# Optimization experiments

Measured on AMD Instinct MI355X. Metric: run time of the kernel, lower is better.

Reference implementation:

```python
import jax, jax.numpy as jnp
import numpy as np

B, T, C = 2, 4096, 768
H = 12
D = C // H  # head_dim = 64

def setup_inputs() -> dict:
    key = jax.random.key(0)
    ks = jax.random.split(key, 5)
    s = 1.0 / np.sqrt(C)
    return {
        "x": jax.random.normal(ks[0], (B, T, C), dtype=jnp.float32),
        "qkv_w": jax.random.normal(ks[1], (C, 3 * C), dtype=jnp.float32) * s,
        "qkv_b": jax.random.normal(ks[2], (3 * C,), dtype=jnp.float32) * 0.02,
        "out_w": jax.random.normal(ks[3], (C, C), dtype=jnp.float32) * s,
        "out_b": jax.random.normal(ks[4], (C,), dtype=jnp.float32) * 0.02,
    }

def reference(x, qkv_w, qkv_b, out_w, out_b):
    b, t, c = x.shape
    qkv = x @ qkv_w + qkv_b                      # [B,T,3C]
    q, k, v = jnp.split(qkv, 3, axis=-1)
    # [B,T,C] -> [B,H,T,D]
    q = q.reshape(b, t, H, D).transpose(0, 2, 1, 3)
    k = k.reshape(b, t, H, D).transpose(0, 2, 1, 3)
    v = v.reshape(b, t, H, D).transpose(0, 2, 1, 3)
    scale = 1.0 / np.sqrt(D)
    attn = jnp.einsum('bhqd,bhkd->bhqk', q, k) * scale  # [B,H,T,T]
    causal = jnp.tril(jnp.ones((t, t), dtype=bool))
    attn = jnp.where(causal, attn, -jnp.inf)
    attn = jax.nn.softmax(attn, axis=-1)
    y = jnp.einsum('bhqk,bhkd->bhqd', attn, v)           # [B,H,T,D]
    y = y.transpose(0, 2, 1, 3).reshape(b, t, c)
    return y @ out_w + out_b
```

## Files before the change

kernel.cpp:

```cpp
#include <hip/hip_runtime.h>
#include <hip/hip_bf16.h>

#define T_SEQ 4096
#define C_DIM 768
#define H_NUM 12
#define D_HEAD 64
#define N3    2304
#define BHN   24

typedef __bf16 bf16x8 __attribute__((ext_vector_type(8)));
typedef float  f32x4  __attribute__((ext_vector_type(4)));

__device__ inline unsigned short f2b(float f) {
    unsigned int x = __float_as_uint(f);
    unsigned int r = (x + 0x7FFFu + ((x >> 16) & 1u)) >> 16;
    return (unsigned short)r;
}

__device__ inline unsigned int pack_trunc(float lo, float hi) {
    return __builtin_amdgcn_perm(__float_as_uint(hi), __float_as_uint(lo), 0x07060302u);
}

__device__ inline void load_lds16(const unsigned short* g, unsigned short* l) {
    __builtin_amdgcn_global_load_lds(
        (const __attribute__((address_space(1))) unsigned int*)(g),
        (__attribute__((address_space(3))) unsigned int*)(l),
        16, 0, 0);
}

__device__ inline void transpose_tile(const float* __restrict__ in,
                                      unsigned short* __restrict__ out,
                                      unsigned short* Ts, int k0, int n0,
                                      int R, int Cc, int tid)
{
    #pragma unroll
    for (int it = 0; it < 4; ++it) {
        int idx = tid + it * 256;
        int r = idx >> 4, c4 = idx & 15;
        float4 v = *reinterpret_cast<const float4*>(&in[(size_t)(k0 + r) * Cc + n0 + c4 * 4]);
        Ts[(c4 * 4 + 0) * 72 + r] = f2b(v.x);
        Ts[(c4 * 4 + 1) * 72 + r] = f2b(v.y);
        Ts[(c4 * 4 + 2) * 72 + r] = f2b(v.z);
        Ts[(c4 * 4 + 3) * 72 + r] = f2b(v.w);
    }
    __syncthreads();
    #pragma unroll
    for (int it = 0; it < 2; ++it) {
        int idx = tid + it * 256;
        int row = idx >> 3, ch = idx & 7;
        *reinterpret_cast<uint4*>(&out[(size_t)(n0 + row) * R + k0 + ch * 8]) =
            *reinterpret_cast<const uint4*>(&Ts[row * 72 + ch * 8]);
    }
}

__global__ __launch_bounds__(256) void prep(
    const float* __restrict__ x, const float* __restrict__ qkv_w,
    const float* __restrict__ out_w,
    unsigned short* __restrict__ xb, unsigned short* __restrict__ wtq,
    unsigned short* __restrict__ wto)
{
    __shared__ unsigned short Ts[64 * 72];
    const int b = blockIdx.x, tid = threadIdx.x;
    if (b < 6144) {
        int idx = b * 256 + tid;
        float4 v = reinterpret_cast<const float4*>(x)[idx];
        ushort4 u;
        u.x = f2b(v.x); u.y = f2b(v.y); u.z = f2b(v.z); u.w = f2b(v.w);
        reinterpret_cast<ushort4*>(xb)[idx] = u;
    } else if (b < 6576) {
        int bb = b - 6144;
        transpose_tile(qkv_w, wtq, Ts, (bb % 12) * 64, (bb / 12) * 64, C_DIM, N3, tid);
    } else {
        int bb = b - 6576;
        transpose_tile(out_w, wto, Ts, (bb % 12) * 64, (bb / 12) * 64, C_DIM, C_DIM, tid);
    }
}

__global__ __launch_bounds__(256) void qkv_gemm(
    const unsigned short* __restrict__ xb, const unsigned short* __restrict__ wt,
    const float* __restrict__ bias,
    unsigned short* __restrict__ Q, unsigned short* __restrict__ K,
    unsigned short* __restrict__ Vt)
{
    __shared__ unsigned short SH[128 * 128];
    unsigned short* As = SH;
    unsigned short* Bs = SH + 128 * 64;
    const int tid  = threadIdx.x;
    const int m0   = blockIdx.x * 128;
    const int n0   = blockIdx.y * 128;
    const int lane = tid & 63;
    const int wv   = tid >> 6;
    const int wr   = wv >> 1, wc = wv & 1;
    const int quad = lane >> 4;
    const int lr   = lane & 15;
    const int srow = lane >> 3;
    const int dch  = (lane & 7) ^ srow;

    f32x4 acc[4][4] = {};

    for (int kk = 0; kk < C_DIM; kk += 64) {
        __syncthreads();
        #pragma unroll
        for (int i = 0; i < 4; ++i) {
            int inst = wv * 4 + i;
            int r = inst * 8 + srow;
            load_lds16(xb + (size_t)(m0 + r) * C_DIM + kk + dch * 8, As + inst * 512);
            load_lds16(wt + (size_t)(n0 + r) * C_DIM + kk + dch * 8, Bs + inst * 512);
        }
        __syncthreads();
        #pragma unroll
        for (int k2 = 0; k2 < 2; ++k2) {
            bf16x8 af[4], bf[4];
            #pragma unroll
            for (int mt = 0; mt < 4; ++mt)
                af[mt] = *reinterpret_cast<const bf16x8*>(
                    &As[(wr * 64 + mt * 16 + lr) * 64 + (((k2 * 4 + quad) ^ (lr & 7)) * 8)]);
            #pragma unroll
            for (int nt = 0; nt < 4; ++nt)
                bf[nt] = *reinterpret_cast<const bf16x8*>(
                    &Bs[(wc * 64 + nt * 16 + lr) * 64 + (((k2 * 4 + quad) ^ (lr & 7)) * 8)]);
            #pragma unroll
            for (int mt = 0; mt < 4; ++mt)
                #pragma unroll
                for (int nt = 0; nt < 4; ++nt)
                    acc[mt][nt] = __builtin_amdgcn_mfma_f32_16x16x32_bf16(af[mt], bf[nt], acc[mt][nt], 0, 0, 0);
        }
    }

    const int whichblk = n0 / C_DIM;
    if (whichblk == 2) {
        __syncthreads();
        #pragma unroll
        for (int nt = 0; nt < 4; ++nt) {
            int dp = wc * 64 + nt * 16 + lr;
            float bj = bias[n0 + dp];
            #pragma unroll
            for (int mt = 0; mt < 4; ++mt) {
                int t0 = wr * 64 + mt * 16 + quad * 4;
                ushort4 u;
                u.x = f2b(acc[mt][nt][0] + bj);
                u.y = f2b(acc[mt][nt][1] + bj);
                u.z = f2b(acc[mt][nt][2] + bj);
                u.w = f2b(acc[mt][nt][3] + bj);
                int cs = (t0 >> 2) ^ ((dp & 15) << 1);
                *reinterpret_cast<ushort4*>(&SH[dp * 128 + cs * 4]) = u;
            }
        }
        __syncthreads();
        const int bb = m0 >> 12;
        const int t_base = m0 & 4095;
        const int h_base = (n0 - 2 * C_DIM) >> 6;
        #pragma unroll
        for (int i = 0; i < 8; ++i) {
            int idx = i * 256 + tid;
            int row = idx >> 4, cc = idx & 15;
            int pc = ((2 * cc) ^ ((row & 15) << 1)) * 4;
            uint4 val = *reinterpret_cast<const uint4*>(&SH[row * 128 + pc]);
            int head = h_base + (row >> 6);
            int d = row & 63;
            *reinterpret_cast<uint4*>(
                &Vt[((size_t)(bb * H_NUM + head) * D_HEAD + d) * T_SEQ + t_base + cc * 8]) = val;
        }
    } else {
        const int head0 = ((n0 % C_DIM) + wc * 64) >> 6;
        #pragma unroll
        for (int nt = 0; nt < 4; ++nt) {
            int d = nt * 16 + lr;
            float bj = bias[n0 + wc * 64 + nt * 16 + lr];
            #pragma unroll
            for (int mt = 0; mt < 4; ++mt) {
                #pragma unroll
                for (int reg = 0; reg < 4; ++reg) {
                    int i = m0 + wr * 64 + mt * 16 + quad * 4 + reg;
                    int bb = i >> 12, t = i & 4095;
                    float val = acc[mt][nt][reg] + bj;
                    size_t base = (size_t)(bb * H_NUM + head0) * T_SEQ + t;
                    if (whichblk == 0)
                        Q[base * D_HEAD + d] = f2b(val * 0.18033688011f);
                    else
                        K[base * D_HEAD + d] = f2b(val);
                }
            }
        }
    }
}

__global__ __launch_bounds__(256, 3) void flash_attn(
    const unsigned short* __restrict__ Q, const unsigned short* __restrict__ K,
    const unsigned short* __restrict__ Vt, unsigned short* __restrict__ Y)
{
    __shared__ unsigned short Ks[2][64 * 64];
    __shared__ unsigned short Vs[2][64 * 64];
    __shared__ unsigned short Ps[2][64 * 72];
    const int tid  = threadIdx.x;
    const int lane = tid & 63;
    const int wv   = tid >> 6;
    const int quad = lane >> 4;
    const int lr   = lane & 15;
    const int srow = lane >> 3;
    const int dch  = (lane & 7) ^ srow;

    const int bid = blockIdx.x;
    const int qt  = 31 - (bid / BHN);
    const int bh  = bid % BHN;
    const int q0  = qt * 128;
    const int diag0 = 2 * qt;
    const int last  = diag0 + 1;

    const unsigned short* Qb = Q  + (size_t)bh * T_SEQ * D_HEAD;
    const unsigned short* Kb = K  + (size_t)bh * T_SEQ * D_HEAD;
    const unsigned short* Vb = Vt + (size_t)bh * D_HEAD * T_SEQ;

    bf16x8 bQ[2][2];
    #pragma unroll
    for (int h = 0; h < 2; ++h)
        #pragma unroll
        for (int k2 = 0; k2 < 2; ++k2)
            bQ[h][k2] = *reinterpret_cast<const bf16x8*>(
                &Qb[(size_t)(q0 + h * 64 + wv * 16 + lr) * D_HEAD + k2 * 32 + quad * 8]);

    bf16x8 ones;
    #pragma unroll
    for (int i = 0; i < 8; ++i) ones[i] = (__bf16)1.0f;
    const f32x4 zf = {};

    f32x4 oacc[2][4] = {};
    f32x4 lacc[2] = {};

    unsigned short* Pw0 = &Ps[0][(wv * 16) * 72];
    unsigned short* Pw1 = &Ps[1][(wv * 16) * 72];

    #pragma unroll
    for (int i = 0; i < 2; ++i) {
        int inst = wv * 2 + i;
        int r = inst * 8 + srow;
        load_lds16(Kb + (size_t)r * D_HEAD + dch * 8, Ks[0] + inst * 512);
        load_lds16(Vb + (size_t)r * T_SEQ + dch * 8, Vs[0] + inst * 512);
    }

    for (int kt = 0; kt <= last; ++kt) {
        const int buf = kt & 1;
        __syncthreads();

        if (kt < last) {
            #pragma unroll
            for (int i = 0; i < 2; ++i) {
                int inst = wv * 2 + i;
                int r = inst * 8 + srow;
                load_lds16(Kb + (size_t)((kt + 1) * 64 + r) * D_HEAD + dch * 8,
                           Ks[buf ^ 1] + inst * 512);
                load_lds16(Vb + (size_t)r * T_SEQ + (kt + 1) * 64 + dch * 8,
                           Vs[buf ^ 1] + inst * 512);
            }
        }

        const bool doh0 = (kt <= diag0);

        bf16x8 aK[4][2];
        #pragma unroll
        for (int mt = 0; mt < 4; ++mt)
            #pragma unroll
            for (int k2 = 0; k2 < 2; ++k2)
                aK[mt][k2] = *reinterpret_cast<const bf16x8*>(
                    &Ks[buf][(mt * 16 + lr) * 64 + (((k2 * 4 + quad) ^ (lr & 7)) * 8)]);

        f32x4 st0[4], st1[4];
        #pragma unroll
        for (int mt = 0; mt < 4; ++mt) {
            st1[mt] = __builtin_amdgcn_mfma_f32_16x16x32_bf16(aK[mt][0], bQ[1][0], zf, 0, 0, 0);
            st1[mt] = __builtin_amdgcn_mfma_f32_16x16x32_bf16(aK[mt][1], bQ[1][1], st1[mt], 0, 0, 0);
        }
        if (doh0) {
            #pragma unroll
            for (int mt = 0; mt < 4; ++mt) {
                st0[mt] = __builtin_amdgcn_mfma_f32_16x16x32_bf16(aK[mt][0], bQ[0][0], zf, 0, 0, 0);
                st0[mt] = __builtin_amdgcn_mfma_f32_16x16x32_bf16(aK[mt][1], bQ[0][1], st0[mt], 0, 0, 0);
            }
        }

        if (kt == diag0) {
            int qg = q0 + wv * 16 + lr;
            #pragma unroll
            for (int mt = 0; mt < 4; ++mt)
                #pragma unroll
                for (int reg = 0; reg < 4; ++reg)
                    if (kt * 64 + mt * 16 + quad * 4 + reg > qg) st0[mt][reg] = -INFINITY;
        }
        if (kt == last) {
            int qg = q0 + 64 + wv * 16 + lr;
            #pragma unroll
            for (int mt = 0; mt < 4; ++mt)
                #pragma unroll
                for (int reg = 0; reg < 4; ++reg)
                    if (kt * 64 + mt * 16 + quad * 4 + reg > qg) st1[mt][reg] = -INFINITY;
        }

        #pragma unroll
        for (int mt = 0; mt < 4; ++mt) {
            #pragma unroll
            for (int reg = 0; reg < 4; ++reg)
                st1[mt][reg] = __builtin_amdgcn_exp2f(st1[mt][reg]);
            uint2 u;
            u.x = pack_trunc(st1[mt][0], st1[mt][1]);
            u.y = pack_trunc(st1[mt][2], st1[mt][3]);
            *reinterpret_cast<uint2*>(&Pw1[lr * 72 + mt * 16 + quad * 4]) = u;
        }
        if (doh0) {
            #pragma unroll
            for (int mt = 0; mt < 4; ++mt) {
                #pragma unroll
                for (int reg = 0; reg < 4; ++reg)
                    st0[mt][reg] = __builtin_amdgcn_exp2f(st0[mt][reg]);
                uint2 u;
                u.x = pack_trunc(st0[mt][0], st0[mt][1]);
                u.y = pack_trunc(st0[mt][2], st0[mt][3]);
                *reinterpret_cast<uint2*>(&Pw0[lr * 72 + mt * 16 + quad * 4]) = u;
            }
        }

        bf16x8 aV[4][2];
        #pragma unroll
        for (int mt = 0; mt < 4; ++mt)
            #pragma unroll
            for (int k2 = 0; k2 < 2; ++k2)
                aV[mt][k2] = *reinterpret_cast<const bf16x8*>(
                    &Vs[buf][(mt * 16 + lr) * 64 + (((k2 * 4 + quad) ^ (lr & 7)) * 8)]);

        if (doh0) {
            bf16x8 bP0 = *reinterpret_cast<const bf16x8*>(&Pw0[lr * 72 + quad * 8]);
            bf16x8 bP1 = *reinterpret_cast<const bf16x8*>(&Pw0[lr * 72 + 32 + quad * 8]);
            #pragma unroll
            for (int dt = 0; dt < 4; ++dt) {
                oacc[0][dt] = __builtin_amdgcn_mfma_f32_16x16x32_bf16(aV[dt][0], bP0, oacc[0][dt], 0, 0, 0);
                oacc[0][dt] = __builtin_amdgcn_mfma_f32_16x16x32_bf16(aV[dt][1], bP1, oacc[0][dt], 0, 0, 0);
            }
            lacc[0] = __builtin_amdgcn_mfma_f32_16x16x32_bf16(ones, bP0, lacc[0], 0, 0, 0);
            lacc[0] = __builtin_amdgcn_mfma_f32_16x16x32_bf16(ones, bP1, lacc[0], 0, 0, 0);
        }
        {
            bf16x8 bP0 = *reinterpret_cast<const bf16x8*>(&Pw1[lr * 72 + quad * 8]);
            bf16x8 bP1 = *reinterpret_cast<const bf16x8*>(&Pw1[lr * 72 + 32 + quad * 8]);
            #pragma unroll
            for (int dt = 0; dt < 4; ++dt) {
                oacc[1][dt] = __builtin_amdgcn_mfma_f32_16x16x32_bf16(aV[dt][0], bP0, oacc[1][dt], 0, 0, 0);
                oacc[1][dt] = __builtin_amdgcn_mfma_f32_16x16x32_bf16(aV[dt][1], bP1, oacc[1][dt], 0, 0, 0);
            }
            lacc[1] = __builtin_amdgcn_mfma_f32_16x16x32_bf16(ones, bP0, lacc[1], 0, 0, 0);
            lacc[1] = __builtin_amdgcn_mfma_f32_16x16x32_bf16(ones, bP1, lacc[1], 0, 0, 0);
        }
    }

    const int bb = bh / H_NUM, hh = bh % H_NUM;
    #pragma unroll
    for (int h = 0; h < 2; ++h) {
        float inv = 1.f / lacc[h][0];
        int q = q0 + h * 64 + wv * 16 + lr;
        #pragma unroll
        for (int dt = 0; dt < 4; ++dt) {
            ushort4 u;
            u.x = f2b(oacc[h][dt][0] * inv);
            u.y = f2b(oacc[h][dt][1] * inv);
            u.z = f2b(oacc[h][dt][2] * inv);
            u.w = f2b(oacc[h][dt][3] * inv);
            *reinterpret_cast<ushort4*>(
                &Y[(size_t)(bb * T_SEQ + q) * C_DIM + hh * 64 + dt * 16 + quad * 4]) = u;
        }
    }
}

__global__ __launch_bounds__(256) void out_gemm(
    const unsigned short* __restrict__ Y, const unsigned short* __restrict__ wt,
    const float* __restrict__ bias, float* __restrict__ out)
{
    __shared__ unsigned short As[128 * 64];
    __shared__ unsigned short Bs[64 * 64];
    const int tid  = threadIdx.x;
    const int m0   = blockIdx.x * 128;
    const int n0   = blockIdx.y * 64;
    const int lane = tid & 63;
    const int wv   = tid >> 6;
    const int wr   = wv >> 1, wc = wv & 1;
    const int quad = lane >> 4;
    const int lr   = lane & 15;
    const int srow = lane >> 3;
    const int dch  = (lane & 7) ^ srow;

    f32x4 acc[4][2] = {};

    for (int kk = 0; kk < C_DIM; kk += 64) {
        __syncthreads();
        #pragma unroll
        for (int i = 0; i < 4; ++i) {
            int inst = wv * 4 + i;
            int r = inst * 8 + srow;
            load_lds16(Y + (size_t)(m0 + r) * C_DIM + kk + dch * 8, As + inst * 512);
        }
        #pragma unroll
        for (int i = 0; i < 2; ++i) {
            int inst = wv * 2 + i;
            int r = inst * 8 + srow;
            load_lds16(wt + (size_t)(n0 + r) * C_DIM + kk + dch * 8, Bs + inst * 512);
        }
        __syncthreads();
        #pragma unroll
        for (int k2 = 0; k2 < 2; ++k2) {
            bf16x8 af[4], bf[2];
            #pragma unroll
            for (int mt = 0; mt < 4; ++mt)
                af[mt] = *reinterpret_cast<const bf16x8*>(
                    &As[(wr * 64 + mt * 16 + lr) * 64 + (((k2 * 4 + quad) ^ (lr & 7)) * 8)]);
            #pragma unroll
            for (int nt = 0; nt < 2; ++nt)
                bf[nt] = *reinterpret_cast<const bf16x8*>(
                    &Bs[(wc * 32 + nt * 16 + lr) * 64 + (((k2 * 4 + quad) ^ (lr & 7)) * 8)]);
            #pragma unroll
            for (int mt = 0; mt < 4; ++mt)
                #pragma unroll
                for (int nt = 0; nt < 2; ++nt)
                    acc[mt][nt] = __builtin_amdgcn_mfma_f32_16x16x32_bf16(af[mt], bf[nt], acc[mt][nt], 0, 0, 0);
        }
    }

    #pragma unroll
    for (int nt = 0; nt < 2; ++nt) {
        int j = n0 + wc * 32 + nt * 16 + lr;
        float bj = bias[j];
        #pragma unroll
        for (int mt = 0; mt < 4; ++mt)
            #pragma unroll
            for (int reg = 0; reg < 4; ++reg) {
                int i = m0 + wr * 64 + mt * 16 + quad * 4 + reg;
                out[(size_t)i * C_DIM + j] = acc[mt][nt][reg] + bj;
            }
    }
}

extern "C" void kernel_launch(void* const* d_in, const int* in_sizes, int n_in,
                              void* d_out, int out_size, void* d_ws, size_t ws_size,
                              hipStream_t stream) {
    const float* x     = (const float*)d_in[0];
    const float* qkv_w = (const float*)d_in[1];
    const float* qkv_b = (const float*)d_in[2];
    const float* out_w = (const float*)d_in[3];
    const float* out_b = (const float*)d_in[4];
    float* out = (float*)d_out;

    unsigned short* xb  = (unsigned short*)d_ws;
    unsigned short* wtq = xb  + (size_t)8192 * 768;
    unsigned short* wto = wtq + (size_t)2304 * 768;
    unsigned short* Qs  = wto + (size_t)768 * 768;
    unsigned short* Kg  = Qs  + (size_t)BHN * T_SEQ * D_HEAD;
    unsigned short* Vt  = Kg  + (size_t)BHN * T_SEQ * D_HEAD;
    unsigned short* Y   = xb;

    prep      <<<6720, 256, 0, stream>>>(x, qkv_w, out_w, xb, wtq, wto);
    qkv_gemm  <<<dim3(64, 18), 256, 0, stream>>>(xb, wtq, qkv_b, Qs, Kg, Vt);
    flash_attn<<<dim3(32 * BHN), 256, 0, stream>>>(Qs, Kg, Vt, Y);
    out_gemm  <<<dim3(64, 12), 256, 0, stream>>>(Y, wto, out_b, out);
}
```

Measured before the change: 230.5 us.

## Keep P in registers using 16x16x16 MFMA, dropping LDS P round-trip

```diff
diff --git a/kernel.cpp b/kernel.cpp
--- a/kernel.cpp
+++ b/kernel.cpp
@@ -10,6 +10,7 @@
 
 typedef __bf16 bf16x8 __attribute__((ext_vector_type(8)));
 typedef float  f32x4  __attribute__((ext_vector_type(4)));
+typedef short  s16x4  __attribute__((ext_vector_type(4)));
 
 __device__ inline unsigned short f2b(float f) {
     unsigned int x = __float_as_uint(f);
@@ -185,13 +186,12 @@
     }
 }
 
-__global__ __launch_bounds__(256, 3) void flash_attn(
+__global__ __launch_bounds__(256, 4) void flash_attn(
     const unsigned short* __restrict__ Q, const unsigned short* __restrict__ K,
     const unsigned short* __restrict__ Vt, unsigned short* __restrict__ Y)
 {
     __shared__ unsigned short Ks[2][64 * 64];
     __shared__ unsigned short Vs[2][64 * 64];
-    __shared__ unsigned short Ps[2][64 * 72];
     const int tid  = threadIdx.x;
     const int lane = tid & 63;
     const int wv   = tid >> 6;
@@ -219,16 +219,13 @@
             bQ[h][k2] = *reinterpret_cast<const bf16x8*>(
                 &Qb[(size_t)(q0 + h * 64 + wv * 16 + lr) * D_HEAD + k2 * 32 + quad * 8]);
 
-    bf16x8 ones;
-    #pragma unroll
-    for (int i = 0; i < 8; ++i) ones[i] = (__bf16)1.0f;
+    s16x4 ones4;
+    #pragma unroll
+    for (int i = 0; i < 4; ++i) ones4[i] = (short)0x3F80;
     const f32x4 zf = {};
 
     f32x4 oacc[2][4] = {};
     f32x4 lacc[2] = {};
-
-    unsigned short* Pw0 = &Ps[0][(wv * 16) * 72];
-    unsigned short* Pw1 = &Ps[1][(wv * 16) * 72];
 
     #pragma unroll
     for (int i = 0; i < 2; ++i) {
@@ -256,25 +253,18 @@
 
         const bool doh0 = (kt <= diag0);
 
-        bf16x8 aK[4][2];
-        #pragma unroll
-        for (int mt = 0; mt < 4; ++mt)
-            #pragma unroll
-            for (int k2 = 0; k2 < 2; ++k2)
-                aK[mt][k2] = *reinterpret_cast<const bf16x8*>(
-                    &Ks[buf][(mt * 16 + lr) * 64 + (((k2 * 4 + quad) ^ (lr & 7)) * 8)]);
-
         f32x4 st0[4], st1[4];
         #pragma unroll
         for (int mt = 0; mt < 4; ++mt) {
-            st1[mt] = __builtin_amdgcn_mfma_f32_16x16x32_bf16(aK[mt][0], bQ[1][0], zf, 0, 0, 0);
-            st1[mt] = __builtin_amdgcn_mfma_f32_16x16x32_bf16(aK[mt][1], bQ[1][1], st1[mt], 0, 0, 0);
-        }
-        if (doh0) {
-            #pragma unroll
-            for (int mt = 0; mt < 4; ++mt) {
-                st0[mt] = __builtin_amdgcn_mfma_f32_16x16x32_bf16(aK[mt][0], bQ[0][0], zf, 0, 0, 0);
-                st0[mt] = __builtin_amdgcn_mfma_f32_16x16x32_bf16(aK[mt][1], bQ[0][1], st0[mt], 0, 0, 0);
+            bf16x8 aK0 = *reinterpret_cast<const bf16x8*>(
+                &Ks[buf][(mt * 16 + lr) * 64 + ((quad ^ (lr & 7)) * 8)]);
+            bf16x8 aK1 = *reinterpret_cast<const bf16x8*>(
+                &Ks[buf][(mt * 16 + lr) * 64 + (((4 + quad) ^ (lr & 7)) * 8)]);
+            st1[mt] = __builtin_amdgcn_mfma_f32_16x16x32_bf16(aK0, bQ[1][0], zf, 0, 0, 0);
+            st1[mt] = __builtin_amdgcn_mfma_f32_16x16x32_bf16(aK1, bQ[1][1], st1[mt], 0, 0, 0);
+            if (doh0) {
+                st0[mt] = __builtin_amdgcn_mfma_f32_16x16x32_bf16(aK0, bQ[0][0], zf, 0, 0, 0);
+                st0[mt] = __builtin_amdgcn_mfma_f32_16x16x32_bf16(aK1, bQ[0][1], st0[mt], 0, 0, 0);
             }
         }
 
@@ -295,6 +285,7 @@
                     if (kt * 64 + mt * 16 + quad * 4 + reg > qg) st1[mt][reg] = -INFINITY;
         }
 
+        s16x4 bP1v[4], bP0v[4];
         #pragma unroll
         for (int mt = 0; mt < 4; ++mt) {
             #pragma unroll
@@ -303,7 +294,7 @@
             uint2 u;
             u.x = pack_trunc(st1[mt][0], st1[mt][1]);
             u.y = pack_trunc(st1[mt][2], st1[mt][3]);
-            *reinterpret_cast<uint2*>(&Pw1[lr * 72 + mt * 16 + quad * 4]) = u;
+            bP1v[mt] = __builtin_bit_cast(s16x4, u);
         }
         if (doh0) {
             #pragma unroll
@@ -314,39 +305,28 @@
                 uint2 u;
                 u.x = pack_trunc(st0[mt][0], st0[mt][1]);
                 u.y = pack_trunc(st0[mt][2], st0[mt][3]);
-                *reinterpret_cast<uint2*>(&Pw0[lr * 72 + mt * 16 + quad * 4]) = u;
-            }
-        }
-
-        bf16x8 aV[4][2];
-        #pragma unroll
-        for (int mt = 0; mt < 4; ++mt)
-            #pragma unroll
-            for (int k2 = 0; k2 < 2; ++k2)
-                aV[mt][k2] = *reinterpret_cast<const bf16x8*>(
-                    &Vs[buf][(mt * 16 + lr) * 64 + (((k2 * 4 + quad) ^ (lr & 7)) * 8)]);
-
-        if (doh0) {
-            bf16x8 bP0 = *reinterpret_cast<const bf16x8*>(&Pw0[lr * 72 + quad * 8]);
-            bf16x8 bP1 = *reinterpret_cast<const bf16x8*>(&Pw0[lr * 72 + 32 + quad * 8]);
-            #pragma unroll
-            for (int dt = 0; dt < 4; ++dt) {
-                oacc[0][dt] = __builtin_amdgcn_mfma_f32_16x16x32_bf16(aV[dt][0], bP0, oacc[0][dt], 0, 0, 0);
-                oacc[0][dt] = __builtin_amdgcn_mfma_f32_16x16x32_bf16(aV[dt][1], bP1, oacc[0][dt], 0, 0, 0);
-            }
-            lacc[0] = __builtin_amdgcn_mfma_f32_16x16x32_bf16(ones, bP0, lacc[0], 0, 0, 0);
-            lacc[0] = __builtin_amdgcn_mfma_f32_16x16x32_bf16(ones, bP1, lacc[0], 0, 0, 0);
-        }
-        {
-            bf16x8 bP0 = *reinterpret_cast<const bf16x8*>(&Pw1[lr * 72 + quad * 8]);
-            bf16x8 bP1 = *reinterpret_cast<const bf16x8*>(&Pw1[lr * 72 + 32 + quad * 8]);
-            #pragma unroll
-            for (int dt = 0; dt < 4; ++dt) {
-                oacc[1][dt] = __builtin_amdgcn_mfma_f32_16x16x32_bf16(aV[dt][0], bP0, oacc[1][dt], 0, 0, 0);
-                oacc[1][dt] = __builtin_amdgcn_mfma_f32_16x16x32_bf16(aV[dt][1], bP1, oacc[1][dt], 0, 0, 0);
-            }
-            lacc[1] = __builtin_amdgcn_mfma_f32_16x16x32_bf16(ones, bP0, lacc[1], 0, 0, 0);
-            lacc[1] = __builtin_amdgcn_mfma_f32_16x16x32_bf16(ones, bP1, lacc[1], 0, 0, 0);
+                bP0v[mt] = __builtin_bit_cast(s16x4, u);
+            }
+        }
+
+        #pragma unroll
+        for (int kb = 0; kb < 4; ++kb) {
+            s16x4 aV[4];
+            #pragma unroll
+            for (int dt = 0; dt < 4; ++dt)
+                aV[dt] = *reinterpret_cast<const s16x4*>(
+                    &Vs[buf][(dt * 16 + lr) * 64 +
+                             (((2 * kb + (quad >> 1)) ^ (lr & 7)) * 8) + (quad & 1) * 4]);
+            #pragma unroll
+            for (int dt = 0; dt < 4; ++dt)
+                oacc[1][dt] = __builtin_amdgcn_mfma_f32_16x16x16bf16_1k(aV[dt], bP1v[kb], oacc[1][dt], 0, 0, 0);
+            lacc[1] = __builtin_amdgcn_mfma_f32_16x16x16bf16_1k(ones4, bP1v[kb], lacc[1], 0, 0, 0);
+            if (doh0) {
+                #pragma unroll
+                for (int dt = 0; dt < 4; ++dt)
+                    oacc[0][dt] = __builtin_amdgcn_mfma_f32_16x16x16bf16_1k(aV[dt], bP0v[kb], oacc[0][dt], 0, 0, 0);
+                lacc[0] = __builtin_amdgcn_mfma_f32_16x16x16bf16_1k(ones4, bP0v[kb], lacc[0], 0, 0, 0);
+            }
         }
     }
 
```

Result: slower. 240.5 us (+4.3%).

## Balance causal attention work by splitting long query tiles across blocks

Applied to the files above, without the earlier changes.

```diff
diff --git a/kernel.cpp b/kernel.cpp
--- a/kernel.cpp
+++ b/kernel.cpp
@@ -187,7 +187,8 @@
 
 __global__ __launch_bounds__(256, 3) void flash_attn(
     const unsigned short* __restrict__ Q, const unsigned short* __restrict__ K,
-    const unsigned short* __restrict__ Vt, unsigned short* __restrict__ Y)
+    const unsigned short* __restrict__ Vt, unsigned short* __restrict__ Y,
+    float* __restrict__ pO, float* __restrict__ pl)
 {
     __shared__ unsigned short Ks[2][64 * 64];
     __shared__ unsigned short Vs[2][64 * 64];
@@ -201,170 +202,239 @@
     const int dch  = (lane & 7) ^ srow;
 
     const int bid = blockIdx.x;
-    const int qt  = 31 - (bid / BHN);
+    const int ip  = bid / BHN;
     const int bh  = bid % BHN;
-    const int q0  = qt * 128;
-    const int diag0 = 2 * qt;
-    const int last  = diag0 + 1;
 
     const unsigned short* Qb = Q  + (size_t)bh * T_SEQ * D_HEAD;
     const unsigned short* Kb = K  + (size_t)bh * T_SEQ * D_HEAD;
     const unsigned short* Vb = Vt + (size_t)bh * D_HEAD * T_SEQ;
 
-    bf16x8 bQ[2][2];
-    #pragma unroll
-    for (int h = 0; h < 2; ++h)
-        #pragma unroll
-        for (int k2 = 0; k2 < 2; ++k2)
-            bQ[h][k2] = *reinterpret_cast<const bf16x8*>(
-                &Qb[(size_t)(q0 + h * 64 + wv * 16 + lr) * D_HEAD + k2 * 32 + quad * 8]);
+    int njob, jqt[2], jk0[2], jk1[2], jpart[2];
+    if (ip < 16) {
+        njob = 2;
+        jqt[0] = ip;      jk0[0] = 0; jk1[0] = 2 * ip + 2;  jpart[0] = 0;
+        jqt[1] = 31 - ip; jk0[1] = 0; jk1[1] = 31 - 2 * ip; jpart[1] = 1;
+    } else {
+        njob = 1;
+        jqt[0] = ip; jk0[0] = 2 * ip - 31; jk1[0] = 2 * ip + 2; jpart[0] = 2;
+    }
 
     bf16x8 ones;
     #pragma unroll
     for (int i = 0; i < 8; ++i) ones[i] = (__bf16)1.0f;
     const f32x4 zf = {};
 
-    f32x4 oacc[2][4] = {};
-    f32x4 lacc[2] = {};
-
     unsigned short* Pw0 = &Ps[0][(wv * 16) * 72];
     unsigned short* Pw1 = &Ps[1][(wv * 16) * 72];
-
+    const int bb = bh / H_NUM, hh = bh % H_NUM;
+
+    int buf = 0;
+    {
+        int kt = jk0[0];
+        #pragma unroll
+        for (int i = 0; i < 2; ++i) {
+            int inst = wv * 2 + i;
+            int r = inst * 8 + srow;
+            load_lds16(Kb + (size_t)(kt * 64 + r) * D_HEAD + dch * 8, Ks[0] + inst * 512);
+            load_lds16(Vb + (size_t)r * T_SEQ + kt * 64 + dch * 8, Vs[0] + inst * 512);
+        }
+    }
+
+    for (int job = 0; job < njob; ++job) {
+        const int qt = jqt[job];
+        const int q0 = qt * 128;
+        const int diag0 = 2 * qt;
+        const int lastk = 2 * qt + 1;
+        const int k0 = jk0[job], k1 = jk1[job];
+
+        bf16x8 bQ[2][2];
+        #pragma unroll
+        for (int h = 0; h < 2; ++h)
+            #pragma unroll
+            for (int k2 = 0; k2 < 2; ++k2)
+                bQ[h][k2] = *reinterpret_cast<const bf16x8*>(
+                    &Qb[(size_t)(q0 + h * 64 + wv * 16 + lr) * D_HEAD + k2 * 32 + quad * 8]);
+
+        f32x4 oacc[2][4] = {};
+        f32x4 lacc[2] = {};
+
+        for (int kt = k0; kt < k1; ++kt) {
+            __syncthreads();
+
+            int nkt = (kt + 1 < k1) ? (kt + 1) : ((job + 1 < njob) ? jk0[job + 1] : -1);
+            if (nkt >= 0) {
+                #pragma unroll
+                for (int i = 0; i < 2; ++i) {
+                    int inst = wv * 2 + i;
+                    int r = inst * 8 + srow;
+                    load_lds16(Kb + (size_t)(nkt * 64 + r) * D_HEAD + dch * 8,
+                               Ks[buf ^ 1] + inst * 512);
+                    load_lds16(Vb + (size_t)r * T_SEQ + nkt * 64 + dch * 8,
+                               Vs[buf ^ 1] + inst * 512);
+                }
+            }
+
+            const bool doh0 = (kt <= diag0);
+
+            bf16x8 aK[4][2];
+            #pragma unroll
+            for (int mt = 0; mt < 4; ++mt)
+                #pragma unroll
+                for (int k2 = 0; k2 < 2; ++k2)
+                    aK[mt][k2] = *reinterpret_cast<const bf16x8*>(
+                        &Ks[buf][(mt * 16 + lr) * 64 + (((k2 * 4 + quad) ^ (lr & 7)) * 8)]);
+
+            f32x4 st0[4], st1[4];
+            #pragma unroll
+            for (int mt = 0; mt < 4; ++mt) {
+                st1[mt] = __builtin_amdgcn_mfma_f32_16x16x32_bf16(aK[mt][0], bQ[1][0], zf, 0, 0, 0);
+                st1[mt] = __builtin_amdgcn_mfma_f32_16x16x32_bf16(aK[mt][1], bQ[1][1], st1[mt], 0, 0, 0);
+            }
+            if (doh0) {
+                #pragma unroll
+                for (int mt = 0; mt < 4; ++mt) {
+                    st0[mt] = __builtin_amdgcn_mfma_f32_16x16x32_bf16(aK[mt][0], bQ[0][0], zf, 0, 0, 0);
+                    st0[mt] = __builtin_amdgcn_mfma_f32_16x16x32_bf16(aK[mt][1], bQ[0][1], st0[mt], 0, 0, 0);
+                }
+            }
+
+            if (kt == diag0) {
+                int qg = q0 + wv * 16 + lr;
+                #pragma unroll
+                for (int mt = 0; mt < 4; ++mt)
+                    #pragma unroll
+                    for (int reg = 0; reg < 4; ++reg)
+                        if (kt * 64 + mt * 16 + quad * 4 + reg > qg) st0[mt][reg] = -INFINITY;
+            }
+            if (kt == lastk) {
+                int qg = q0 + 64 + wv * 16 + lr;
+                #pragma unroll
+                for (int mt = 0; mt < 4; ++mt)
+                    #pragma unroll
+                    for (int reg = 0; reg < 4; ++reg)
+                        if (kt * 64 + mt * 16 + quad * 4 + reg > qg) st1[mt][reg] = -INFINITY;
+            }
+
+            #pragma unroll
+            for (int mt = 0; mt < 4; ++mt) {
+                #pragma unroll
+                for (int reg = 0; reg < 4; ++reg)
+                    st1[mt][reg] = __builtin_amdgcn_exp2f(st1[mt][reg]);
+                uint2 u;
+                u.x = pack_trunc(st1[mt][0], st1[mt][1]);
+                u.y = pack_trunc(st1[mt][2], st1[mt][3]);
+                *reinterpret_cast<uint2*>(&Pw1[lr * 72 + mt * 16 + quad * 4]) = u;
+            }
+            if (doh0) {
+                #pragma unroll
+                for (int mt = 0; mt < 4; ++mt) {
+                    #pragma unroll
+                    for (int reg = 0; reg < 4; ++reg)
+                        st0[mt][reg] = __builtin_amdgcn_exp2f(st0[mt][reg]);
+                    uint2 u;
+                    u.x = pack_trunc(st0[mt][0], st0[mt][1]);
+                    u.y = pack_trunc(st0[mt][2], st0[mt][3]);
+                    *reinterpret_cast<uint2*>(&Pw0[lr * 72 + mt * 16 + quad * 4]) = u;
+                }
+            }
+
+            bf16x8 aV[4][2];
+            #pragma unroll
+            for (int mt = 0; mt < 4; ++mt)
+                #pragma unroll
+                for (int k2 = 0; k2 < 2; ++k2)
+                    aV[mt][k2] = *reinterpret_cast<const bf16x8*>(
+                        &Vs[buf][(mt * 16 + lr) * 64 + (((k2 * 4 + quad) ^ (lr & 7)) * 8)]);
+
+            if (doh0) {
+                bf16x8 bP0 = *reinterpret_cast<const bf16x8*>(&Pw0[lr * 72 + quad * 8]);
+                bf16x8 bP1 = *reinterpret_cast<const bf16x8*>(&Pw0[lr * 72 + 32 + quad * 8]);
+                #pragma unroll
+                for (int dt = 0; dt < 4; ++dt) {
+                    oacc[0][dt] = __builtin_amdgcn_mfma_f32_16x16x32_bf16(aV[dt][0], bP0, oacc[0][dt], 0, 0, 0);
+                    oacc[0][dt] = __builtin_amdgcn_mfma_f32_16x16x32_bf16(aV[dt][1], bP1, oacc[0][dt], 0, 0, 0);
+                }
+                lacc[0] = __builtin_amdgcn_mfma_f32_16x16x32_bf16(ones, bP0, lacc[0], 0, 0, 0);
+                lacc[0] = __builtin_amdgcn_mfma_f32_16x16x32_bf16(ones, bP1, lacc[0], 0, 0, 0);
+            }
+            {
+                bf16x8 bP0 = *reinterpret_cast<const bf16x8*>(&Pw1[lr * 72 + quad * 8]);
+                bf16x8 bP1 = *reinterpret_cast<const bf16x8*>(&Pw1[lr * 72 + 32 + quad * 8]);
+                #pragma unroll
+                for (int dt = 0; dt < 4; ++dt) {
+                    oacc[1][dt] = __builtin_amdgcn_mfma_f32_16x16x32_bf16(aV[dt][0], bP0, oacc[1][dt], 0, 0, 0);
+                    oacc[1][dt] = __builtin_amdgcn_mfma_f32_16x16x32_bf16(aV[dt][1], bP1, oacc[1][dt], 0, 0, 0);
+                }
+                lacc[1] = __builtin_amdgcn_mfma_f32_16x16x32_bf16(ones, bP0, lacc[1], 0, 0, 0);
+                lacc[1] = __builtin_amdgcn_mfma_f32_16x16x32_bf16(ones, bP1, lacc[1], 0, 0, 0);
+            }
+
+            buf ^= 1;
+        }
+
+        if (jpart[job] == 0) {
+            #pragma unroll
+            for (int h = 0; h < 2; ++h) {
+                float inv = 1.f / lacc[h][0];
+                int q = q0 + h * 64 + wv * 16 + lr;
+                #pragma unroll
+                for (int dt = 0; dt < 4; ++dt) {
+                    ushort4 u;
+                    u.x = f2b(oacc[h][dt][0] * inv);
+                    u.y = f2b(oacc[h][dt][1] * inv);
+                    u.z = f2b(oacc[h][dt][2] * inv);
+                    u.w = f2b(oacc[h][dt][3] * inv);
+                    *reinterpret_cast<ushort4*>(
+                        &Y[(size_t)(bb * T_SEQ + q) * C_DIM + hh * 64 + dt * 16 + quad * 4]) = u;
+                }
+            }
+        } else {
+            const int slot = jpart[job] - 1;
+            const int iH = 31 - qt;
+            const size_t s = (size_t)slot * 384 + (size_t)bh * 16 + iH;
+            float* po  = pO + s * 8192;
+            float* plp = pl + s * 128;
+            #pragma unroll
+            for (int h = 0; h < 2; ++h) {
+                int q = h * 64 + wv * 16 + lr;
+                if (quad == 0) plp[q] = lacc[h][0];
+                #pragma unroll
+                for (int dt = 0; dt < 4; ++dt)
+                    *reinterpret_cast<f32x4*>(&po[(size_t)q * 64 + dt * 16 + quad * 4]) = oacc[h][dt];
+            }
+        }
+    }
+}
+
+__global__ __launch_bounds__(256) void combine(
+    const float* __restrict__ pO, const float* __restrict__ pl,
+    unsigned short* __restrict__ Y)
+{
+    const int s   = blockIdx.x;
+    const int tid = threadIdx.x;
+    const int bh  = s / 16, iH = s % 16;
+    const int qt  = 31 - iH;
+    const int bb  = bh / H_NUM, hh = bh % H_NUM;
+    const int q0  = qt * 128;
+    const float* a  = pO + (size_t)s * 8192;
+    const float* b  = pO + (size_t)(384 + s) * 8192;
+    const float* la = pl + (size_t)s * 128;
+    const float* lb = pl + (size_t)(384 + s) * 128;
     #pragma unroll
-    for (int i = 0; i < 2; ++i) {
-        int inst = wv * 2 + i;
-        int r = inst * 8 + srow;
-        load_lds16(Kb + (size_t)r * D_HEAD + dch * 8, Ks[0] + inst * 512);
-        load_lds16(Vb + (size_t)r * T_SEQ + dch * 8, Vs[0] + inst * 512);
-    }
-
-    for (int kt = 0; kt <= last; ++kt) {
-        const int buf = kt & 1;
-        __syncthreads();
-
-        if (kt < last) {
-            #pragma unroll
-            for (int i = 0; i < 2; ++i) {
-                int inst = wv * 2 + i;
-                int r = inst * 8 + srow;
-                load_lds16(Kb + (size_t)((kt + 1) * 64 + r) * D_HEAD + dch * 8,
-                           Ks[buf ^ 1] + inst * 512);
-                load_lds16(Vb + (size_t)r * T_SEQ + (kt + 1) * 64 + dch * 8,
-                           Vs[buf ^ 1] + inst * 512);
-            }
-        }
-
-        const bool doh0 = (kt <= diag0);
-
-        bf16x8 aK[4][2];
-        #pragma unroll
-        for (int mt = 0; mt < 4; ++mt)
-            #pragma unroll
-            for (int k2 = 0; k2 < 2; ++k2)
-                aK[mt][k2] = *reinterpret_cast<const bf16x8*>(
-                    &Ks[buf][(mt * 16 + lr) * 64 + (((k2 * 4 + quad) ^ (lr & 7)) * 8)]);
-
-        f32x4 st0[4], st1[4];
-        #pragma unroll
-        for (int mt = 0; mt < 4; ++mt) {
-            st1[mt] = __builtin_amdgcn_mfma_f32_16x16x32_bf16(aK[mt][0], bQ[1][0], zf, 0, 0, 0);
-            st1[mt] = __builtin_amdgcn_mfma_f32_16x16x32_bf16(aK[mt][1], bQ[1][1], st1[mt], 0, 0, 0);
-        }
-        if (doh0) {
-            #pragma unroll
-            for (int mt = 0; mt < 4; ++mt) {
-                st0[mt] = __builtin_amdgcn_mfma_f32_16x16x32_bf16(aK[mt][0], bQ[0][0], zf, 0, 0, 0);
-                st0[mt] = __builtin_amdgcn_mfma_f32_16x16x32_bf16(aK[mt][1], bQ[0][1], st0[mt], 0, 0, 0);
-            }
-        }
-
-        if (kt == diag0) {
-            int qg = q0 + wv * 16 + lr;
-            #pragma unroll
-            for (int mt = 0; mt < 4; ++mt)
-                #pragma unroll
-                for (int reg = 0; reg < 4; ++reg)
-                    if (kt * 64 + mt * 16 + quad * 4 + reg > qg) st0[mt][reg] = -INFINITY;
-        }
-        if (kt == last) {
-            int qg = q0 + 64 + wv * 16 + lr;
-            #pragma unroll
-            for (int mt = 0; mt < 4; ++mt)
-                #pragma unroll
-                for (int reg = 0; reg < 4; ++reg)
-                    if (kt * 64 + mt * 16 + quad * 4 + reg > qg) st1[mt][reg] = -INFINITY;
-        }
-
-        #pragma unroll
-        for (int mt = 0; mt < 4; ++mt) {
-            #pragma unroll
-            for (int reg = 0; reg < 4; ++reg)
-                st1[mt][reg] = __builtin_amdgcn_exp2f(st1[mt][reg]);
-            uint2 u;
-            u.x = pack_trunc(st1[mt][0], st1[mt][1]);
-            u.y = pack_trunc(st1[mt][2], st1[mt][3]);
-            *reinterpret_cast<uint2*>(&Pw1[lr * 72 + mt * 16 + quad * 4]) = u;
-        }
-        if (doh0) {
-            #pragma unroll
-            for (int mt = 0; mt < 4; ++mt) {
-                #pragma unroll
-                for (int reg = 0; reg < 4; ++reg)
-                    st0[mt][reg] = __builtin_amdgcn_exp2f(st0[mt][reg]);
-                uint2 u;
-                u.x = pack_trunc(st0[mt][0], st0[mt][1]);
-                u.y = pack_trunc(st0[mt][2], st0[mt][3]);
-                *reinterpret_cast<uint2*>(&Pw0[lr * 72 + mt * 16 + quad * 4]) = u;
-            }
-        }
-
-        bf16x8 aV[4][2];
-        #pragma unroll
-        for (int mt = 0; mt < 4; ++mt)
-            #pragma unroll
-            for (int k2 = 0; k2 < 2; ++k2)
-                aV[mt][k2] = *reinterpret_cast<const bf16x8*>(
-                    &Vs[buf][(mt * 16 + lr) * 64 + (((k2 * 4 + quad) ^ (lr & 7)) * 8)]);
-
-        if (doh0) {
-            bf16x8 bP0 = *reinterpret_cast<const bf16x8*>(&Pw0[lr * 72 + quad * 8]);
-            bf16x8 bP1 = *reinterpret_cast<const bf16x8*>(&Pw0[lr * 72 + 32 + quad * 8]);
-            #pragma unroll
-            for (int dt = 0; dt < 4; ++dt) {
-                oacc[0][dt] = __builtin_amdgcn_mfma_f32_16x16x32_bf16(aV[dt][0], bP0, oacc[0][dt], 0, 0, 0);
-                oacc[0][dt] = __builtin_amdgcn_mfma_f32_16x16x32_bf16(aV[dt][1], bP1, oacc[0][dt], 0, 0, 0);
-            }
-            lacc[0] = __builtin_amdgcn_mfma_f32_16x16x32_bf16(ones, bP0, lacc[0], 0, 0, 0);
-            lacc[0] = __builtin_amdgcn_mfma_f32_16x16x32_bf16(ones, bP1, lacc[0], 0, 0, 0);
-        }
-        {
-            bf16x8 bP0 = *reinterpret_cast<const bf16x8*>(&Pw1[lr * 72 + quad * 8]);
-            bf16x8 bP1 = *reinterpret_cast<const bf16x8*>(&Pw1[lr * 72 + 32 + quad * 8]);
-            #pragma unroll
-            for (int dt = 0; dt < 4; ++dt) {
-                oacc[1][dt] = __builtin_amdgcn_mfma_f32_16x16x32_bf16(aV[dt][0], bP0, oacc[1][dt], 0, 0, 0);
-                oacc[1][dt] = __builtin_amdgcn_mfma_f32_16x16x32_bf16(aV[dt][1], bP1, oacc[1][dt], 0, 0, 0);
-            }
-            lacc[1] = __builtin_amdgcn_mfma_f32_16x16x32_bf16(ones, bP0, lacc[1], 0, 0, 0);
-            lacc[1] = __builtin_amdgcn_mfma_f32_16x16x32_bf16(ones, bP1, lacc[1], 0, 0, 0);
-        }
-    }
-
-    const int bb = bh / H_NUM, hh = bh % H_NUM;
-    #pragma unroll
-    for (int h = 0; h < 2; ++h) {
-        float inv = 1.f / lacc[h][0];
-        int q = q0 + h * 64 + wv * 16 + lr;
-        #pragma unroll
-        for (int dt = 0; dt < 4; ++dt) {
-            ushort4 u;
-            u.x = f2b(oacc[h][dt][0] * inv);
-            u.y = f2b(oacc[h][dt][1] * inv);
-            u.z = f2b(oacc[h][dt][2] * inv);
-            u.w = f2b(oacc[h][dt][3] * inv);
-            *reinterpret_cast<ushort4*>(
-                &Y[(size_t)(bb * T_SEQ + q) * C_DIM + hh * 64 + dt * 16 + quad * 4]) = u;
-        }
+    for (int j = 0; j < 8; ++j) {
+        int idx = tid + j * 256;
+        int f = idx * 4;
+        int q = f >> 6, d0 = f & 63;
+        float4 va = *reinterpret_cast<const float4*>(&a[f]);
+        float4 vb = *reinterpret_cast<const float4*>(&b[f]);
+        float inv = 1.f / (la[q] + lb[q]);
+        ushort4 u;
+        u.x = f2b((va.x + vb.x) * inv);
+        u.y = f2b((va.y + vb.y) * inv);
+        u.z = f2b((va.z + vb.z) * inv);
+        u.w = f2b((va.w + vb.w) * inv);
+        *reinterpret_cast<ushort4*>(
+            &Y[(size_t)(bb * T_SEQ + q0 + q) * C_DIM + hh * 64 + d0]) = u;
     }
 }
 
@@ -451,10 +521,13 @@
     unsigned short* Qs  = wto + (size_t)768 * 768;
     unsigned short* Kg  = Qs  + (size_t)BHN * T_SEQ * D_HEAD;
     unsigned short* Vt  = Kg  + (size_t)BHN * T_SEQ * D_HEAD;
+    float*          pO  = (float*)(Vt + (size_t)BHN * T_SEQ * D_HEAD);
+    float*          pl  = pO + (size_t)2 * 384 * 8192;
     unsigned short* Y   = xb;
 
     prep      <<<6720, 256, 0, stream>>>(x, qkv_w, out_w, xb, wtq, wto);
     qkv_gemm  <<<dim3(64, 18), 256, 0, stream>>>(xb, wtq, qkv_b, Qs, Kg, Vt);
-    flash_attn<<<dim3(32 * BHN), 256, 0, stream>>>(Qs, Kg, Vt, Y);
+    flash_attn<<<dim3(32 * BHN), 256, 0, stream>>>(Qs, Kg, Vt, Y, pO, pl);
+    combine   <<<384, 256, 0, stream>>>(pO, pl, Y);
     out_gemm  <<<dim3(64, 12), 256, 0, stream>>>(Y, wto, out_b, out);
 }
```

Measured after the change: 224.8 us. 2.5% less time.
